# Performance work log

Hardware: AMD Instinct MI355X
Metric: run time of the kernel (lower is better)

Reference implementation:

```python
import jax, jax.numpy as jnp
from jax import lax
import numpy as np

B, T, C, H = 2048, 1024, 9, 36  # batch, seq_len, input_size, hidden_size


def setup_inputs() -> dict:
    key = jax.random.key(0)
    ks = jax.random.split(key, 4)
    x = jax.random.normal(ks[0], (B, T, C), dtype=jnp.float32)
    # torch GRU param shapes: weight_ih (3H, C), weight_hh (3H, H), biases (3H,)
    w_ih = jax.random.normal(ks[1], (3 * H, C), dtype=jnp.float32) * (1.0 / np.sqrt(C))
    w_hh = jax.random.normal(ks[2], (3 * H, H), dtype=jnp.float32) * (1.0 / np.sqrt(H))
    b_ih = jnp.zeros((3 * H,), dtype=jnp.float32)
    b_hh = jnp.zeros((3 * H,), dtype=jnp.float32)
    w_head = jax.random.normal(ks[3], (1, H), dtype=jnp.float32) * (1.0 / np.sqrt(H))
    b_head = jnp.zeros((1,), dtype=jnp.float32)
    return {"x": x, "w_ih": w_ih, "w_hh": w_hh, "b_ih": b_ih, "b_hh": b_hh,
            "w_head": w_head, "b_head": b_head}


def reference(x, w_ih, w_hh, b_ih, b_hh, w_head, b_head):
    """TinyGRUInt8.forward in fp32 (Quant/DeQuant stubs are identity).
    GRU (batch_first, torch gate order r,z,n), take last timestep, Linear head.
    """
    h = w_hh.shape[1]
    # Precompute input contribution to all gates for every timestep: (B,T,3H)
    gx = jnp.einsum('btc,gc->btg', x, w_ih) + b_ih
    gx = jnp.moveaxis(gx, 1, 0)  # (T,B,3H) for scan over time

    def step(h_prev, gxt):
        gh = h_prev @ w_hh.T + b_hh                      # (B,3H)
        r = jax.nn.sigmoid(gxt[:, :h] + gh[:, :h])
        z = jax.nn.sigmoid(gxt[:, h:2 * h] + gh[:, h:2 * h])
        n = jnp.tanh(gxt[:, 2 * h:] + r * gh[:, 2 * h:])
        h_new = (1.0 - z) * n + z * h_prev
        return h_new, None

    h0 = jnp.zeros((x.shape[0], h), dtype=x.dtype)
    h_last, _ = lax.scan(step, h0, gx)                   # last output == final hidden
    return h_last @ w_head.T + b_head                    # (B,1)
```

## Files before the change

### kernel.cpp

```cpp
#include <hip/hip_runtime.h>

typedef float     v2f __attribute__((ext_vector_type(2)));
typedef _Float16  v2h __attribute__((ext_vector_type(2)));
typedef unsigned int uint;

#define BB 2048
#define TT 1024
#define CC 9
#define HH 36
#define CSTEPS 64
#define CF (CSTEPS * CC)
#define NCH (TT / CSTEPS)

__device__ __forceinline__ void pin2f(v2f& v) {
    uint64_t t = __builtin_bit_cast(uint64_t, v);
    asm volatile("" : "+v"(t));
    v = __builtin_bit_cast(v2f, t);
}
__device__ __forceinline__ void pinh(v2h& v) {
    uint t = __builtin_bit_cast(uint, v);
    asm volatile("" : "+v"(t));
    v = __builtin_bit_cast(v2h, t);
}

__device__ __forceinline__ void gload4(const float* g, float* l) {
    __builtin_amdgcn_global_load_lds(
        (const __attribute__((address_space(1))) unsigned int*)g,
        (__attribute__((address_space(3))) unsigned int*)l,
        4, 0, 0);
}

__global__ __launch_bounds__(64)
__attribute__((amdgpu_waves_per_eu(2, 2)))
void gru_kernel(
    const float* __restrict__ x,
    const float* __restrict__ w_ih,
    const float* __restrict__ w_hh,
    const float* __restrict__ b_ih,
    const float* __restrict__ b_hh,
    const float* __restrict__ w_head,
    const float* __restrict__ b_head,
    float* __restrict__ out)
{
    const int b = blockIdx.x;
    const int j = threadIdx.x;

    __shared__ __align__(16) _Float16 hbuf16[64];
    __shared__ __align__(16) float xlds[2][CF];

    const int jj = (j < HH) ? j : 0;
    v2h wrh[18], wzh[18], wnh[18];
    v2f wri[4], wzi[4], wni[4];
    float wri8, wzi8, wni8, br, bz, bni, bnh;
    {
        const float* pr = w_hh + (size_t)jj * HH;
        const float* pz = w_hh + (size_t)(HH + jj) * HH;
        const float* pn = w_hh + (size_t)(2 * HH + jj) * HH;
#pragma unroll
        for (int k = 0; k < 18; ++k) {
            wrh[k] = (v2h){(_Float16)pr[2*k], (_Float16)pr[2*k+1]};
            wzh[k] = (v2h){(_Float16)pz[2*k], (_Float16)pz[2*k+1]};
            wnh[k] = (v2h){(_Float16)pn[2*k], (_Float16)pn[2*k+1]};
        }
        const float* qr = w_ih + (size_t)jj * CC;
        const float* qz = w_ih + (size_t)(HH + jj) * CC;
        const float* qn = w_ih + (size_t)(2 * HH + jj) * CC;
#pragma unroll
        for (int p = 0; p < 4; ++p) {
            wri[p] = (v2f){qr[2*p], qr[2*p+1]};
            wzi[p] = (v2f){qz[2*p], qz[2*p+1]};
            wni[p] = (v2f){qn[2*p], qn[2*p+1]};
        }
        wri8 = qr[8]; wzi8 = qz[8]; wni8 = qn[8];
        br  = b_ih[jj] + b_hh[jj];
        bz  = b_ih[HH + jj] + b_hh[HH + jj];
        bni = b_ih[2 * HH + jj];
        bnh = b_hh[2 * HH + jj];
    }
#pragma unroll
    for (int k = 0; k < 18; ++k) { pinh(wrh[k]); pinh(wzh[k]); pinh(wnh[k]); }
#pragma unroll
    for (int p = 0; p < 4; ++p) { pin2f(wri[p]); pin2f(wzi[p]); pin2f(wni[p]); }
    asm volatile("" : "+v"(wri8), "+v"(wzi8), "+v"(wni8));
    asm volatile("" : "+v"(br), "+v"(bz), "+v"(bni), "+v"(bnh));

    const float* xg = x + (size_t)b * (TT * CC);

#pragma unroll
    for (int k = 0; k < 9; ++k) gload4(xg + k * 64 + j, &xlds[0][k * 64]);

    v2h h2[18];
#pragma unroll
    for (int k = 0; k < 18; ++k) h2[k] = (v2h){(_Float16)0.f, (_Float16)0.f};
    float h_own = 0.f;

    for (int c = 0; c < NCH; ++c) {
        asm volatile("s_waitcnt vmcnt(0)" ::: "memory");
        __builtin_amdgcn_sched_barrier(0);
        if (c + 1 < NCH) {
            const float* src = xg + (size_t)(c + 1) * CF;
            float* dst = &xlds[(c + 1) & 1][0];
#pragma unroll
            for (int k = 0; k < 9; ++k) gload4(src + k * 64 + j, dst + k * 64);
        }
        const float* xc = &xlds[c & 1][0];

#pragma unroll 2
        for (int s = 0; s < CSTEPS; ++s) {
            const float* xs = xc + s * CC;
            float xv[CC];
#pragma unroll
            for (int cc = 0; cc < CC; ++cc) xv[cc] = xs[cc];

            v2f axr = (v2f){br,  0.f};
            v2f axz = (v2f){bz,  0.f};
            v2f axn = (v2f){bni, 0.f};
#pragma unroll
            for (int p = 0; p < 4; ++p) {
                v2f xp2 = (v2f){xv[2*p], xv[2*p+1]};
                axr = __builtin_elementwise_fma(wri[p], xp2, axr);
                axz = __builtin_elementwise_fma(wzi[p], xp2, axz);
                axn = __builtin_elementwise_fma(wni[p], xp2, axn);
            }
            float sr = fmaf(wri8, xv[8], axr.x + axr.y);
            float sz = fmaf(wzi8, xv[8], axz.x + axz.y);
            float sn = fmaf(wni8, xv[8], axn.x + axn.y);
            float gn = bnh;

#pragma unroll
            for (int k = 0; k < 18; ++k) {
                sr = __builtin_amdgcn_fdot2(wrh[k], h2[k], sr, false);
                sz = __builtin_amdgcn_fdot2(wzh[k], h2[k], sz, false);
                gn = __builtin_amdgcn_fdot2(wnh[k], h2[k], gn, false);
            }

            float r = __builtin_amdgcn_rcpf(1.f + __expf(-sr));
            float z = __builtin_amdgcn_rcpf(1.f + __expf(-sz));
            float a = sn + r * gn;
            float n = 1.f - 2.f * __builtin_amdgcn_rcpf(__expf(2.f * a) + 1.f);
            h_own = z * (h_own - n) + n;

            hbuf16[j] = (_Float16)h_own;
            {
#pragma unroll
                for (int q = 0; q < 4; ++q) {
                    uint4 t4 = ((const uint4*)hbuf16)[q];
                    h2[4*q+0] = __builtin_bit_cast(v2h, t4.x);
                    h2[4*q+1] = __builtin_bit_cast(v2h, t4.y);
                    h2[4*q+2] = __builtin_bit_cast(v2h, t4.z);
                    h2[4*q+3] = __builtin_bit_cast(v2h, t4.w);
                }
                uint2 t2 = ((const uint2*)hbuf16)[8];
                h2[16] = __builtin_bit_cast(v2h, t2.x);
                h2[17] = __builtin_bit_cast(v2h, t2.y);
            }
        }
    }

    float whead = (j < HH) ? w_head[j] : 0.f;
    float v = (j < HH) ? h_own * whead : 0.f;
#pragma unroll
    for (int off = 32; off; off >>= 1) v += __shfl_down(v, off);
    if (j == 0) out[b] = v + b_head[0];
}

extern "C" void kernel_launch(void* const* d_in, const int* in_sizes, int n_in,
                              void* d_out, int out_size, void* d_ws, size_t ws_size,
                              hipStream_t stream) {
    const float* x      = (const float*)d_in[0];
    const float* w_ih   = (const float*)d_in[1];
    const float* w_hh   = (const float*)d_in[2];
    const float* b_ih   = (const float*)d_in[3];
    const float* b_hh   = (const float*)d_in[4];
    const float* w_head = (const float*)d_in[5];
    const float* b_head = (const float*)d_in[6];
    float* out = (float*)d_out;

    gru_kernel<<<BB, 64, 0, stream>>>(x, w_ih, w_hh, b_ih, b_hh,
                                      w_head, b_head, out);
}
```

Measured before the change: 402.9 us.

## Split gate rows across all 64 lanes and exchange pre-activations via LDS

Measured after the change: 411.9 us. 2.2% more time.

```diff
diff --git a/kernel.cpp b/kernel.cpp
--- a/kernel.cpp
+++ b/kernel.cpp
@@ -8,19 +8,26 @@
 #define TT 1024
 #define CC 9
 #define HH 36
+#define G3 108
 #define CSTEPS 64
 #define CF (CSTEPS * CC)
+#define XP 12
 #define NCH (TT / CSTEPS)
 
+__device__ __forceinline__ void lds_fence() {
+    asm volatile("" ::: "memory");
+    __builtin_amdgcn_sched_barrier(0);
+}
+
+__device__ __forceinline__ void pinh(v2h& v) {
+    uint t = __builtin_bit_cast(uint, v);
+    asm volatile("" : "+v"(t));
+    v = __builtin_bit_cast(v2h, t);
+}
 __device__ __forceinline__ void pin2f(v2f& v) {
     uint64_t t = __builtin_bit_cast(uint64_t, v);
     asm volatile("" : "+v"(t));
     v = __builtin_bit_cast(v2f, t);
-}
-__device__ __forceinline__ void pinh(v2h& v) {
-    uint t = __builtin_bit_cast(uint, v);
-    asm volatile("" : "+v"(t));
-    v = __builtin_bit_cast(v2h, t);
 }
 
 __device__ __forceinline__ void gload4(const float* g, float* l) {
@@ -43,51 +50,54 @@
     float* __restrict__ out)
 {
     const int b = blockIdx.x;
-    const int j = threadIdx.x;
-
-    __shared__ __align__(16) _Float16 hbuf16[64];
-    __shared__ __align__(16) float xlds[2][CF];
-
-    const int jj = (j < HH) ? j : 0;
-    v2h wrh[18], wzh[18], wnh[18];
-    v2f wri[4], wzi[4], wni[4];
-    float wri8, wzi8, wni8, br, bz, bni, bnh;
+    const int l = threadIdx.x;
+
+    __shared__ __align__(16) float    fstage[CF];
+    __shared__ __align__(16) float    xpad[CSTEPS * XP];
+    __shared__ __align__(16) float    pbuf[256];
+    __shared__ __align__(16) _Float16 hbuf[40];
+
+    const int i0 = (2 * l     < G3) ? 2 * l     : G3 - 1;
+    const int i1 = (2 * l + 1 < G3) ? 2 * l + 1 : G3 - 1;
+
+    v2h wh0[18], wh1[18];
+    v2f wx0[4], wx1[4];
+    float w80, w81;
+    float bA0, bB0, bA1, bB1;
     {
-        const float* pr = w_hh + (size_t)jj * HH;
-        const float* pz = w_hh + (size_t)(HH + jj) * HH;
-        const float* pn = w_hh + (size_t)(2 * HH + jj) * HH;
+        const float* p0 = w_hh + (size_t)i0 * HH;
+        const float* p1 = w_hh + (size_t)i1 * HH;
 #pragma unroll
         for (int k = 0; k < 18; ++k) {
-            wrh[k] = (v2h){(_Float16)pr[2*k], (_Float16)pr[2*k+1]};
-            wzh[k] = (v2h){(_Float16)pz[2*k], (_Float16)pz[2*k+1]};
-            wnh[k] = (v2h){(_Float16)pn[2*k], (_Float16)pn[2*k+1]};
-        }
-        const float* qr = w_ih + (size_t)jj * CC;
-        const float* qz = w_ih + (size_t)(HH + jj) * CC;
-        const float* qn = w_ih + (size_t)(2 * HH + jj) * CC;
+            wh0[k] = (v2h){(_Float16)p0[2*k], (_Float16)p0[2*k+1]};
+            wh1[k] = (v2h){(_Float16)p1[2*k], (_Float16)p1[2*k+1]};
+        }
+        const float* q0 = w_ih + (size_t)i0 * CC;
+        const float* q1 = w_ih + (size_t)i1 * CC;
 #pragma unroll
         for (int p = 0; p < 4; ++p) {
-            wri[p] = (v2f){qr[2*p], qr[2*p+1]};
-            wzi[p] = (v2f){qz[2*p], qz[2*p+1]};
-            wni[p] = (v2f){qn[2*p], qn[2*p+1]};
-        }
-        wri8 = qr[8]; wzi8 = qz[8]; wni8 = qn[8];
-        br  = b_ih[jj] + b_hh[jj];
-        bz  = b_ih[HH + jj] + b_hh[HH + jj];
-        bni = b_ih[2 * HH + jj];
-        bnh = b_hh[2 * HH + jj];
+            wx0[p] = (v2f){q0[2*p], q0[2*p+1]};
+            wx1[p] = (v2f){q1[2*p], q1[2*p+1]};
+        }
+        w80 = q0[8];
+        w81 = q1[8];
+        const bool n0 = i0 >= 2 * HH, n1 = i1 >= 2 * HH;
+        bA0 = n0 ? b_ih[i0] : (b_ih[i0] + b_hh[i0]);
+        bB0 = n0 ? b_hh[i0] : 0.f;
+        bA1 = n1 ? b_ih[i1] : (b_ih[i1] + b_hh[i1]);
+        bB1 = n1 ? b_hh[i1] : 0.f;
     }
 #pragma unroll
-    for (int k = 0; k < 18; ++k) { pinh(wrh[k]); pinh(wzh[k]); pinh(wnh[k]); }
-#pragma unroll
-    for (int p = 0; p < 4; ++p) { pin2f(wri[p]); pin2f(wzi[p]); pin2f(wni[p]); }
-    asm volatile("" : "+v"(wri8), "+v"(wzi8), "+v"(wni8));
-    asm volatile("" : "+v"(br), "+v"(bz), "+v"(bni), "+v"(bnh));
+    for (int k = 0; k < 18; ++k) { pinh(wh0[k]); pinh(wh1[k]); }
+#pragma unroll
+    for (int p = 0; p < 4; ++p) { pin2f(wx0[p]); pin2f(wx1[p]); }
+    asm volatile("" : "+v"(w80), "+v"(w81));
+    asm volatile("" : "+v"(bA0), "+v"(bB0), "+v"(bA1), "+v"(bB1));
 
     const float* xg = x + (size_t)b * (TT * CC);
 
 #pragma unroll
-    for (int k = 0; k < 9; ++k) gload4(xg + k * 64 + j, &xlds[0][k * 64]);
+    for (int k = 0; k < 9; ++k) gload4(xg + k * 64 + l, &fstage[k * 64]);
 
     v2h h2[18];
 #pragma unroll
@@ -97,71 +107,92 @@
     for (int c = 0; c < NCH; ++c) {
         asm volatile("s_waitcnt vmcnt(0)" ::: "memory");
         __builtin_amdgcn_sched_barrier(0);
+
+        {
+            float xf[9];
+#pragma unroll
+            for (int q = 0; q < 9; ++q) xf[q] = fstage[l * 9 + q];
+            *(float4*)&xpad[l * XP]     = (float4){xf[0], xf[1], xf[2], xf[3]};
+            *(float4*)&xpad[l * XP + 4] = (float4){xf[4], xf[5], xf[6], xf[7]};
+            xpad[l * XP + 8] = xf[8];
+        }
+        lds_fence();
+
         if (c + 1 < NCH) {
             const float* src = xg + (size_t)(c + 1) * CF;
-            float* dst = &xlds[(c + 1) & 1][0];
-#pragma unroll
-            for (int k = 0; k < 9; ++k) gload4(src + k * 64 + j, dst + k * 64);
-        }
-        const float* xc = &xlds[c & 1][0];
+#pragma unroll
+            for (int k = 0; k < 9; ++k) gload4(src + k * 64 + l, &fstage[k * 64]);
+        }
 
 #pragma unroll 2
         for (int s = 0; s < CSTEPS; ++s) {
-            const float* xs = xc + s * CC;
-            float xv[CC];
-#pragma unroll
-            for (int cc = 0; cc < CC; ++cc) xv[cc] = xs[cc];
-
-            v2f axr = (v2f){br,  0.f};
-            v2f axz = (v2f){bz,  0.f};
-            v2f axn = (v2f){bni, 0.f};
-#pragma unroll
-            for (int p = 0; p < 4; ++p) {
-                v2f xp2 = (v2f){xv[2*p], xv[2*p+1]};
-                axr = __builtin_elementwise_fma(wri[p], xp2, axr);
-                axz = __builtin_elementwise_fma(wzi[p], xp2, axz);
-                axn = __builtin_elementwise_fma(wni[p], xp2, axn);
-            }
-            float sr = fmaf(wri8, xv[8], axr.x + axr.y);
-            float sz = fmaf(wzi8, xv[8], axz.x + axz.y);
-            float sn = fmaf(wni8, xv[8], axn.x + axn.y);
-            float gn = bnh;
-
+            float4 xa = *(const float4*)&xpad[s * XP];
+            float4 xb = *(const float4*)&xpad[s * XP + 4];
+            float  x8 = xpad[s * XP + 8];
+            v2f X0 = (v2f){xa.x, xa.y};
+            v2f X1 = (v2f){xa.z, xa.w};
+            v2f X2 = (v2f){xb.x, xb.y};
+            v2f X3 = (v2f){xb.z, xb.w};
+
+            v2f a0 = (v2f){bA0, 0.f};
+            v2f a1 = (v2f){bA1, 0.f};
+            a0 = __builtin_elementwise_fma(wx0[0], X0, a0);
+            a1 = __builtin_elementwise_fma(wx1[0], X0, a1);
+            a0 = __builtin_elementwise_fma(wx0[1], X1, a0);
+            a1 = __builtin_elementwise_fma(wx1[1], X1, a1);
+            a0 = __builtin_elementwise_fma(wx0[2], X2, a0);
+            a1 = __builtin_elementwise_fma(wx1[2], X2, a1);
+            a0 = __builtin_elementwise_fma(wx0[3], X3, a0);
+            a1 = __builtin_elementwise_fma(wx1[3], X3, a1);
+            float ax0 = fmaf(w80, x8, a0.x + a0.y);
+            float ax1 = fmaf(w81, x8, a1.x + a1.y);
+
+            float ah0 = bB0, ah1 = bB1;
 #pragma unroll
             for (int k = 0; k < 18; ++k) {
-                sr = __builtin_amdgcn_fdot2(wrh[k], h2[k], sr, false);
-                sz = __builtin_amdgcn_fdot2(wzh[k], h2[k], sz, false);
-                gn = __builtin_amdgcn_fdot2(wnh[k], h2[k], gn, false);
-            }
-
-            float r = __builtin_amdgcn_rcpf(1.f + __expf(-sr));
-            float z = __builtin_amdgcn_rcpf(1.f + __expf(-sz));
-            float a = sn + r * gn;
-            float n = 1.f - 2.f * __builtin_amdgcn_rcpf(__expf(2.f * a) + 1.f);
-            h_own = z * (h_own - n) + n;
-
-            hbuf16[j] = (_Float16)h_own;
+                ah0 = __builtin_amdgcn_fdot2(wh0[k], h2[k], ah0, false);
+                ah1 = __builtin_amdgcn_fdot2(wh1[k], h2[k], ah1, false);
+            }
+
+            *(float4*)&pbuf[4 * l] = (float4){ax0, ah0, ax1, ah1};
+            lds_fence();
+
+            if (l < HH) {
+                v2f rp = *(const v2f*)&pbuf[2 * l];
+                v2f zp = *(const v2f*)&pbuf[2 * (HH + l)];
+                v2f np = *(const v2f*)&pbuf[2 * (2 * HH + l)];
+                float sr = rp.x + rp.y;
+                float sz = zp.x + zp.y;
+                float r = __builtin_amdgcn_rcpf(1.f + __expf(-sr));
+                float z = __builtin_amdgcn_rcpf(1.f + __expf(-sz));
+                float a = np.x + r * np.y;
+                float n = 1.f - 2.f * __builtin_amdgcn_rcpf(__expf(2.f * a) + 1.f);
+                h_own = z * (h_own - n) + n;
+                hbuf[l] = (_Float16)h_own;
+            }
+            lds_fence();
+
+#pragma unroll
+            for (int q = 0; q < 4; ++q) {
+                uint4 t4 = ((const uint4*)hbuf)[q];
+                h2[4*q+0] = __builtin_bit_cast(v2h, t4.x);
+                h2[4*q+1] = __builtin_bit_cast(v2h, t4.y);
+                h2[4*q+2] = __builtin_bit_cast(v2h, t4.z);
+                h2[4*q+3] = __builtin_bit_cast(v2h, t4.w);
+            }
             {
-#pragma unroll
-                for (int q = 0; q < 4; ++q) {
-                    uint4 t4 = ((const uint4*)hbuf16)[q];
-                    h2[4*q+0] = __builtin_bit_cast(v2h, t4.x);
-                    h2[4*q+1] = __builtin_bit_cast(v2h, t4.y);
-                    h2[4*q+2] = __builtin_bit_cast(v2h, t4.z);
-                    h2[4*q+3] = __builtin_bit_cast(v2h, t4.w);
-                }
-                uint2 t2 = ((const uint2*)hbuf16)[8];
+                uint2 t2 = ((const uint2*)hbuf)[8];
                 h2[16] = __builtin_bit_cast(v2h, t2.x);
                 h2[17] = __builtin_bit_cast(v2h, t2.y);
             }
         }
     }
 
-    float whead = (j < HH) ? w_head[j] : 0.f;
-    float v = (j < HH) ? h_own * whead : 0.f;
+    float whead = (l < HH) ? w_head[l] : 0.f;
+    float v = (l < HH) ? h_own * whead : 0.f;
 #pragma unroll
     for (int off = 32; off; off >>= 1) v += __shfl_down(v, off);
-    if (j == 0) out[b] = v + b_head[0];
+    if (l == 0) out[b] = v + b_head[0];
 }
 
 extern "C" void kernel_launch(void* const* d_in, const int* in_sizes, int n_in,
```

## Process two batch rows per wave to interleave independent recurrences

Applied to the files above, without the earlier changes.

Measured after the change: 508.0 us. 26.1% more time.

```diff
diff --git a/kernel.cpp b/kernel.cpp
--- a/kernel.cpp
+++ b/kernel.cpp
@@ -5,22 +5,30 @@
 typedef unsigned int uint;
 
 #define BB 2048
+#define NBLK (BB / 2)
 #define TT 1024
 #define CC 9
 #define HH 36
-#define CSTEPS 64
+#define CSTEPS 32
 #define CF (CSTEPS * CC)
+#define FPAD 320
+#define XP 12
 #define NCH (TT / CSTEPS)
 
+__device__ __forceinline__ void lds_fence() {
+    asm volatile("" ::: "memory");
+    __builtin_amdgcn_sched_barrier(0);
+}
+
+__device__ __forceinline__ void pinh(v2h& v) {
+    uint t = __builtin_bit_cast(uint, v);
+    asm volatile("" : "+v"(t));
+    v = __builtin_bit_cast(v2h, t);
+}
 __device__ __forceinline__ void pin2f(v2f& v) {
     uint64_t t = __builtin_bit_cast(uint64_t, v);
     asm volatile("" : "+v"(t));
     v = __builtin_bit_cast(v2f, t);
-}
-__device__ __forceinline__ void pinh(v2h& v) {
-    uint t = __builtin_bit_cast(uint, v);
-    asm volatile("" : "+v"(t));
-    v = __builtin_bit_cast(v2h, t);
 }
 
 __device__ __forceinline__ void gload4(const float* g, float* l) {
@@ -31,7 +39,7 @@
 }
 
 __global__ __launch_bounds__(64)
-__attribute__((amdgpu_waves_per_eu(2, 2)))
+__attribute__((amdgpu_waves_per_eu(1, 1)))
 void gru_kernel(
     const float* __restrict__ x,
     const float* __restrict__ w_ih,
@@ -42,126 +50,220 @@
     const float* __restrict__ b_head,
     float* __restrict__ out)
 {
-    const int b = blockIdx.x;
-    const int j = threadIdx.x;
-
-    __shared__ __align__(16) _Float16 hbuf16[64];
-    __shared__ __align__(16) float xlds[2][CF];
-
-    const int jj = (j < HH) ? j : 0;
-    v2h wrh[18], wzh[18], wnh[18];
-    v2f wri[4], wzi[4], wni[4];
-    float wri8, wzi8, wni8, br, bz, bni, bnh;
+    const int bid = blockIdx.x;
+    const int l   = threadIdx.x;
+    const int b0  = 2 * bid;
+    const int b1  = 2 * bid + 1;
+
+    __shared__ __align__(16) float    fstage[2][FPAD];
+    __shared__ __align__(16) float    xpad[2][CSTEPS * XP];
+    __shared__ __align__(16) _Float16 hbuf[2][40];
+
+    const int u = (l < HH) ? l : HH - 1;
+
+    v2h whr[18], whz[18], whn[18];
+    v2f wir[4], wiz[4], win[4];
+    float wir8, wiz8, win8;
+    float bxr, bxz, bxn, bnh;
     {
-        const float* pr = w_hh + (size_t)jj * HH;
-        const float* pz = w_hh + (size_t)(HH + jj) * HH;
-        const float* pn = w_hh + (size_t)(2 * HH + jj) * HH;
+        const float* pr = w_hh + (size_t)u * HH;
+        const float* pz = w_hh + (size_t)(HH + u) * HH;
+        const float* pn = w_hh + (size_t)(2 * HH + u) * HH;
 #pragma unroll
         for (int k = 0; k < 18; ++k) {
-            wrh[k] = (v2h){(_Float16)pr[2*k], (_Float16)pr[2*k+1]};
-            wzh[k] = (v2h){(_Float16)pz[2*k], (_Float16)pz[2*k+1]};
-            wnh[k] = (v2h){(_Float16)pn[2*k], (_Float16)pn[2*k+1]};
-        }
-        const float* qr = w_ih + (size_t)jj * CC;
-        const float* qz = w_ih + (size_t)(HH + jj) * CC;
-        const float* qn = w_ih + (size_t)(2 * HH + jj) * CC;
+            whr[k] = (v2h){(_Float16)pr[2*k], (_Float16)pr[2*k+1]};
+            whz[k] = (v2h){(_Float16)pz[2*k], (_Float16)pz[2*k+1]};
+            whn[k] = (v2h){(_Float16)pn[2*k], (_Float16)pn[2*k+1]};
+        }
+        const float* qr = w_ih + (size_t)u * CC;
+        const float* qz = w_ih + (size_t)(HH + u) * CC;
+        const float* qn = w_ih + (size_t)(2 * HH + u) * CC;
 #pragma unroll
         for (int p = 0; p < 4; ++p) {
-            wri[p] = (v2f){qr[2*p], qr[2*p+1]};
-            wzi[p] = (v2f){qz[2*p], qz[2*p+1]};
-            wni[p] = (v2f){qn[2*p], qn[2*p+1]};
-        }
-        wri8 = qr[8]; wzi8 = qz[8]; wni8 = qn[8];
-        br  = b_ih[jj] + b_hh[jj];
-        bz  = b_ih[HH + jj] + b_hh[HH + jj];
-        bni = b_ih[2 * HH + jj];
-        bnh = b_hh[2 * HH + jj];
-    }
-#pragma unroll
-    for (int k = 0; k < 18; ++k) { pinh(wrh[k]); pinh(wzh[k]); pinh(wnh[k]); }
-#pragma unroll
-    for (int p = 0; p < 4; ++p) { pin2f(wri[p]); pin2f(wzi[p]); pin2f(wni[p]); }
-    asm volatile("" : "+v"(wri8), "+v"(wzi8), "+v"(wni8));
-    asm volatile("" : "+v"(br), "+v"(bz), "+v"(bni), "+v"(bnh));
-
-    const float* xg = x + (size_t)b * (TT * CC);
-
-#pragma unroll
-    for (int k = 0; k < 9; ++k) gload4(xg + k * 64 + j, &xlds[0][k * 64]);
-
-    v2h h2[18];
-#pragma unroll
-    for (int k = 0; k < 18; ++k) h2[k] = (v2h){(_Float16)0.f, (_Float16)0.f};
-    float h_own = 0.f;
+            wir[p] = (v2f){qr[2*p], qr[2*p+1]};
+            wiz[p] = (v2f){qz[2*p], qz[2*p+1]};
+            win[p] = (v2f){qn[2*p], qn[2*p+1]};
+        }
+        wir8 = qr[8]; wiz8 = qz[8]; win8 = qn[8];
+        bxr = b_ih[u] + b_hh[u];
+        bxz = b_ih[HH + u] + b_hh[HH + u];
+        bxn = b_ih[2 * HH + u];
+        bnh = b_hh[2 * HH + u];
+    }
+#pragma unroll
+    for (int k = 0; k < 18; ++k) { pinh(whr[k]); pinh(whz[k]); pinh(whn[k]); }
+#pragma unroll
+    for (int p = 0; p < 4; ++p) { pin2f(wir[p]); pin2f(wiz[p]); pin2f(win[p]); }
+    asm volatile("" : "+v"(wir8), "+v"(wiz8), "+v"(win8));
+    asm volatile("" : "+v"(bxr), "+v"(bxz), "+v"(bxn), "+v"(bnh));
+
+    int offs[5];
+#pragma unroll
+    for (int k = 0; k < 5; ++k) {
+        int idx = k * 64 + l;
+        offs[k] = (idx < CF) ? idx : (CF - 1);
+    }
+
+    const float* xg0 = x + (size_t)b0 * (TT * CC);
+    const float* xg1 = x + (size_t)b1 * (TT * CC);
+
+#pragma unroll
+    for (int k = 0; k < 5; ++k) {
+        gload4(xg0 + offs[k], &fstage[0][k * 64]);
+        gload4(xg1 + offs[k], &fstage[1][k * 64]);
+    }
+
+    v2h h2A[18], h2B[18];
+#pragma unroll
+    for (int k = 0; k < 18; ++k) {
+        h2A[k] = (v2h){(_Float16)0.f, (_Float16)0.f};
+        h2B[k] = (v2h){(_Float16)0.f, (_Float16)0.f};
+    }
+    float hA = 0.f, hB = 0.f;
 
     for (int c = 0; c < NCH; ++c) {
         asm volatile("s_waitcnt vmcnt(0)" ::: "memory");
         __builtin_amdgcn_sched_barrier(0);
+
+        {
+            const int bs = l >> 5;
+            const int s  = l & 31;
+            const float* src = &fstage[bs][s * CC];
+            float xf[9];
+#pragma unroll
+            for (int q = 0; q < 9; ++q) xf[q] = src[q];
+            float* dst = &xpad[bs][s * XP];
+            *(float4*)dst       = (float4){xf[0], xf[1], xf[2], xf[3]};
+            *(float4*)(dst + 4) = (float4){xf[4], xf[5], xf[6], xf[7]};
+            dst[8] = xf[8];
+        }
+        lds_fence();
+
         if (c + 1 < NCH) {
-            const float* src = xg + (size_t)(c + 1) * CF;
-            float* dst = &xlds[(c + 1) & 1][0];
-#pragma unroll
-            for (int k = 0; k < 9; ++k) gload4(src + k * 64 + j, dst + k * 64);
-        }
-        const float* xc = &xlds[c & 1][0];
-
-#pragma unroll 2
+            const float* s0 = xg0 + (size_t)(c + 1) * CF;
+            const float* s1 = xg1 + (size_t)(c + 1) * CF;
+#pragma unroll
+            for (int k = 0; k < 5; ++k) {
+                gload4(s0 + offs[k], &fstage[0][k * 64]);
+                gload4(s1 + offs[k], &fstage[1][k * 64]);
+            }
+        }
+
         for (int s = 0; s < CSTEPS; ++s) {
-            const float* xs = xc + s * CC;
-            float xv[CC];
-#pragma unroll
-            for (int cc = 0; cc < CC; ++cc) xv[cc] = xs[cc];
-
-            v2f axr = (v2f){br,  0.f};
-            v2f axz = (v2f){bz,  0.f};
-            v2f axn = (v2f){bni, 0.f};
-#pragma unroll
-            for (int p = 0; p < 4; ++p) {
-                v2f xp2 = (v2f){xv[2*p], xv[2*p+1]};
-                axr = __builtin_elementwise_fma(wri[p], xp2, axr);
-                axz = __builtin_elementwise_fma(wzi[p], xp2, axz);
-                axn = __builtin_elementwise_fma(wni[p], xp2, axn);
-            }
-            float sr = fmaf(wri8, xv[8], axr.x + axr.y);
-            float sz = fmaf(wzi8, xv[8], axz.x + axz.y);
-            float sn = fmaf(wni8, xv[8], axn.x + axn.y);
-            float gn = bnh;
-
+            const float* xA = &xpad[0][s * XP];
+            const float* xB = &xpad[1][s * XP];
+            float4 a03 = *(const float4*)xA;
+            float4 a47 = *(const float4*)(xA + 4);
+            float  a8  = xA[8];
+            float4 c03 = *(const float4*)xB;
+            float4 c47 = *(const float4*)(xB + 4);
+            float  c8  = xB[8];
+            v2f XA0 = (v2f){a03.x, a03.y}, XA1 = (v2f){a03.z, a03.w};
+            v2f XA2 = (v2f){a47.x, a47.y}, XA3 = (v2f){a47.z, a47.w};
+            v2f XB0 = (v2f){c03.x, c03.y}, XB1 = (v2f){c03.z, c03.w};
+            v2f XB2 = (v2f){c47.x, c47.y}, XB3 = (v2f){c47.z, c47.w};
+
+            v2f tra = (v2f){bxr, 0.f}, tza = (v2f){bxz, 0.f}, tna = (v2f){bxn, 0.f};
+            v2f trb = (v2f){bxr, 0.f}, tzb = (v2f){bxz, 0.f}, tnb = (v2f){bxn, 0.f};
+            tra = __builtin_elementwise_fma(wir[0], XA0, tra);
+            tza = __builtin_elementwise_fma(wiz[0], XA0, tza);
+            tna = __builtin_elementwise_fma(win[0], XA0, tna);
+            trb = __builtin_elementwise_fma(wir[0], XB0, trb);
+            tzb = __builtin_elementwise_fma(wiz[0], XB0, tzb);
+            tnb = __builtin_elementwise_fma(win[0], XB0, tnb);
+            tra = __builtin_elementwise_fma(wir[1], XA1, tra);
+            tza = __builtin_elementwise_fma(wiz[1], XA1, tza);
+            tna = __builtin_elementwise_fma(win[1], XA1, tna);
+            trb = __builtin_elementwise_fma(wir[1], XB1, trb);
+            tzb = __builtin_elementwise_fma(wiz[1], XB1, tzb);
+            tnb = __builtin_elementwise_fma(win[1], XB1, tnb);
+            tra = __builtin_elementwise_fma(wir[2], XA2, tra);
+            tza = __builtin_elementwise_fma(wiz[2], XA2, tza);
+            tna = __builtin_elementwise_fma(win[2], XA2, tna);
+            trb = __builtin_elementwise_fma(wir[2], XB2, trb);
+            tzb = __builtin_elementwise_fma(wiz[2], XB2, tzb);
+            tnb = __builtin_elementwise_fma(win[2], XB2, tnb);
+            tra = __builtin_elementwise_fma(wir[3], XA3, tra);
+            tza = __builtin_elementwise_fma(wiz[3], XA3, tza);
+            tna = __builtin_elementwise_fma(win[3], XA3, tna);
+            trb = __builtin_elementwise_fma(wir[3], XB3, trb);
+            tzb = __builtin_elementwise_fma(wiz[3], XB3, tzb);
+            tnb = __builtin_elementwise_fma(win[3], XB3, tnb);
+            float gxrA = fmaf(wir8, a8, tra.x + tra.y);
+            float gxzA = fmaf(wiz8, a8, tza.x + tza.y);
+            float gxnA = fmaf(win8, a8, tna.x + tna.y);
+            float gxrB = fmaf(wir8, c8, trb.x + trb.y);
+            float gxzB = fmaf(wiz8, c8, tzb.x + tzb.y);
+            float gxnB = fmaf(win8, c8, tnb.x + tnb.y);
+
+            float ahrA = 0.f, ahzA = 0.f, ahnA = bnh;
+            float ahrB = 0.f, ahzB = 0.f, ahnB = bnh;
 #pragma unroll
             for (int k = 0; k < 18; ++k) {
-                sr = __builtin_amdgcn_fdot2(wrh[k], h2[k], sr, false);
-                sz = __builtin_amdgcn_fdot2(wzh[k], h2[k], sz, false);
-                gn = __builtin_amdgcn_fdot2(wnh[k], h2[k], gn, false);
-            }
-
-            float r = __builtin_amdgcn_rcpf(1.f + __expf(-sr));
-            float z = __builtin_amdgcn_rcpf(1.f + __expf(-sz));
-            float a = sn + r * gn;
-            float n = 1.f - 2.f * __builtin_amdgcn_rcpf(__expf(2.f * a) + 1.f);
-            h_own = z * (h_own - n) + n;
-
-            hbuf16[j] = (_Float16)h_own;
+                ahrA = __builtin_amdgcn_fdot2(whr[k], h2A[k], ahrA, false);
+                ahzA = __builtin_amdgcn_fdot2(whz[k], h2A[k], ahzA, false);
+                ahnA = __builtin_amdgcn_fdot2(whn[k], h2A[k], ahnA, false);
+                ahrB = __builtin_amdgcn_fdot2(whr[k], h2B[k], ahrB, false);
+                ahzB = __builtin_amdgcn_fdot2(whz[k], h2B[k], ahzB, false);
+                ahnB = __builtin_amdgcn_fdot2(whn[k], h2B[k], ahnB, false);
+            }
+
+            float srA = gxrA + ahrA, szA = gxzA + ahzA;
+            float rA = __builtin_amdgcn_rcpf(1.f + __expf(-srA));
+            float zA = __builtin_amdgcn_rcpf(1.f + __expf(-szA));
+            float aA = gxnA + rA * ahnA;
+            float nA = 1.f - 2.f * __builtin_amdgcn_rcpf(__expf(2.f * aA) + 1.f);
+            hA = zA * (hA - nA) + nA;
+
+            float srB = gxrB + ahrB, szB = gxzB + ahzB;
+            float rB = __builtin_amdgcn_rcpf(1.f + __expf(-srB));
+            float zB = __builtin_amdgcn_rcpf(1.f + __expf(-szB));
+            float aB = gxnB + rB * ahnB;
+            float nB = 1.f - 2.f * __builtin_amdgcn_rcpf(__expf(2.f * aB) + 1.f);
+            hB = zB * (hB - nB) + nB;
+
+            if (l < HH) {
+                hbuf[0][l] = (_Float16)hA;
+                hbuf[1][l] = (_Float16)hB;
+            }
+            lds_fence();
+
+#pragma unroll
+            for (int q = 0; q < 4; ++q) {
+                uint4 t4 = ((const uint4*)hbuf[0])[q];
+                h2A[4*q+0] = __builtin_bit_cast(v2h, t4.x);
+                h2A[4*q+1] = __builtin_bit_cast(v2h, t4.y);
+                h2A[4*q+2] = __builtin_bit_cast(v2h, t4.z);
+                h2A[4*q+3] = __builtin_bit_cast(v2h, t4.w);
+                uint4 u4 = ((const uint4*)hbuf[1])[q];
+                h2B[4*q+0] = __builtin_bit_cast(v2h, u4.x);
+                h2B[4*q+1] = __builtin_bit_cast(v2h, u4.y);
+                h2B[4*q+2] = __builtin_bit_cast(v2h, u4.z);
+                h2B[4*q+3] = __builtin_bit_cast(v2h, u4.w);
+            }
             {
-#pragma unroll
-                for (int q = 0; q < 4; ++q) {
-                    uint4 t4 = ((const uint4*)hbuf16)[q];
-                    h2[4*q+0] = __builtin_bit_cast(v2h, t4.x);
-                    h2[4*q+1] = __builtin_bit_cast(v2h, t4.y);
-                    h2[4*q+2] = __builtin_bit_cast(v2h, t4.z);
-                    h2[4*q+3] = __builtin_bit_cast(v2h, t4.w);
-                }
-                uint2 t2 = ((const uint2*)hbuf16)[8];
-                h2[16] = __builtin_bit_cast(v2h, t2.x);
-                h2[17] = __builtin_bit_cast(v2h, t2.y);
-            }
-        }
-    }
-
-    float whead = (j < HH) ? w_head[j] : 0.f;
-    float v = (j < HH) ? h_own * whead : 0.f;
-#pragma unroll
-    for (int off = 32; off; off >>= 1) v += __shfl_down(v, off);
-    if (j == 0) out[b] = v + b_head[0];
+                uint2 t2 = ((const uint2*)hbuf[0])[8];
+                h2A[16] = __builtin_bit_cast(v2h, t2.x);
+                h2A[17] = __builtin_bit_cast(v2h, t2.y);
+                uint2 u2 = ((const uint2*)hbuf[1])[8];
+                h2B[16] = __builtin_bit_cast(v2h, u2.x);
+                h2B[17] = __builtin_bit_cast(v2h, u2.y);
+            }
+        }
+    }
+
+    float whead = (l < HH) ? w_head[l] : 0.f;
+    float vA = (l < HH) ? hA * whead : 0.f;
+    float vB = (l < HH) ? hB * whead : 0.f;
+#pragma unroll
+    for (int off = 32; off; off >>= 1) {
+        vA += __shfl_down(vA, off);
+        vB += __shfl_down(vB, off);
+    }
+    if (l == 0) {
+        out[b0] = vA + b_head[0];
+        out[b1] = vB + b_head[0];
+    }
 }
 
 extern "C" void kernel_launch(void* const* d_in, const int* in_sizes, int n_in,
@@ -176,6 +278,6 @@
     const float* b_head = (const float*)d_in[6];
     float* out = (float*)d_out;
 
-    gru_kernel<<<BB, 64, 0, stream>>>(x, w_ih, w_hh, b_ih, b_hh,
-                                      w_head, b_head, out);
-}
+    gru_kernel<<<NBLK, 64, 0, stream>>>(x, w_ih, w_hh, b_ih, b_hh,
+                                        w_head, b_head, out);
+}
```
